# Kernel optimization log

Measured on AMD Instinct MI355X. Metric: run time of the kernel, lower is better.

The kernel has to match this reference:

```python
import jax, jax.numpy as jnp
import numpy as np
import math

C64 = jnp.complex64

def _fftconv_full(a, kern):
    # full linear convolution along last axis (complex), like scipy.signal.fftconvolve
    L = a.shape[-1] + kern.shape[0] - 1
    A = jnp.fft.fft(a, n=L, axis=-1)
    K = jnp.fft.fft(kern.astype(a.dtype), n=L)
    return jnp.fft.ifft(A * K, axis=-1)

def _centered_ifft(f):
    # out[shft] = ifft(f[shft]) * sqrt(N), shft = (arange(N)+fix(N/2)) % N
    N = f.shape[-1]
    shft = (np.arange(N) + int(np.fix(N / 2))) % N
    inv = np.argsort(shft)
    g = jnp.fft.ifft(f[..., shft], axis=-1) * math.sqrt(N)
    return g[..., inv].astype(f.dtype)

def _sincinterp(f):
    # zero-stuff by 2 then sinc-filter; returns length 2N-1 along last axis
    N = f.shape[-1]
    y = jnp.zeros(f.shape[:-1] + (2 * N - 1,), f.dtype).at[..., ::2].set(f)
    kern = jnp.asarray(np.sinc(np.arange(-(2 * N - 3), 2 * N - 2) / 2.0).astype(np.complex64))
    return _fftconv_full(y, kern)[..., 2 * N - 3: 4 * N - 4]

def _frft_chirp(f, a):
    # Ozaktas chirp-convolution discrete FrFT, valid for 0.5 <= a <= 1.5
    N = f.shape[-1]
    alpha = a * math.pi / 2
    tana2, sina = math.tan(alpha / 2), math.sin(alpha)
    fi = _sincinterp(f)                                   # [..., 2N-1]
    pad = jnp.zeros(f.shape[:-1] + (N - 1,), f.dtype)
    fp = jnp.concatenate([pad, fi, pad], axis=-1)         # [..., 4N-3]
    n = np.arange(-2 * N + 2, 2 * N - 1).astype(np.float64)
    chrp = jnp.asarray(np.exp(-1j * math.pi / N * tana2 / 4 * n ** 2).astype(np.complex64))
    fp = chrp * fp
    c = math.pi / N / sina / 4
    m = np.arange(-(4 * N - 4), 4 * N - 3).astype(np.float64)
    kern = jnp.asarray(np.exp(1j * c * m ** 2).astype(np.complex64))
    ret = _fftconv_full(fp, kern)[..., 4 * N - 4: 8 * N - 7] * math.sqrt(c / math.pi)
    ret = chrp * ret
    phase = np.complex64(np.exp(-1j * (1 - a) * math.pi / 4))
    return phase * ret[..., N - 1: 3 * N - 2: 2]          # [..., N]

def _frft_last(f, a):
    # torch branch logic for the a values used here: a=0.5 (fwd), a=-0.5 (inv)
    if a < 0.5:
        f = _centered_ifft(f)
        a = a + 1.0
    return _frft_chirp(f, a)

def _frft2d(x, a):
    t = _frft_last(x, a)                                  # rows: along W
    return jnp.swapaxes(_frft_last(jnp.swapaxes(t, -1, -2), a), -1, -2)  # cols: along H

def _c1x1(x, w, b=None):
    y = jnp.einsum('nchw,oc->nohw', x, w)
    return y if b is None else y + b[None, :, None, None]

def _c3x3(x, w, b):
    y = jax.lax.conv_general_dilated(x, w, (1, 1), 'SAME',
                                     dimension_numbers=('NCHW', 'OIHW', 'NCHW'))
    return y + b[None, :, None, None]

def _forward(x, conv1_w, mag_s_w, mag_s_b, mag_f_w, mag_f_b, mag_w, mag_b,
             pha_w, pha_b, conv_0_w, conv_0_b, conv_1_w, conv_1_b, conv2_w):
    angle = 0.5
    alpha = math.cos(angle * math.pi / 2)
    N, C, H, W = x.shape
    H1, W1 = int(H * alpha), int(W * alpha)
    x1 = _c1x1(x, conv1_w)                                # stride=1 -> downsample is identity
    C1, C0 = C // 4, C // 4 // 3
    x_0, x_05, x_1 = x1[:, :C0], x1[:, C0:C1 - C0], x1[:, C1 - C0:C1]
    h0, w0 = (H - H1) // 2, (W - W1) // 2
    mask1 = jnp.zeros((H, W), jnp.float32).at[h0:h0 + H1, w0:w0 + W1].set(1.0)
    mask2 = 1.0 - mask1
    # fractional Fourier branch
    Fre = _frft2d(x_05.astype(C64), angle)
    mag, pha = jnp.abs(Fre), jnp.angle(Fre)
    mag_out = _c1x1(_c3x3(mag * mask1, mag_s_w, mag_s_b) * mask1
                    + _c1x1(mag * mask2, mag_f_w, mag_f_b) * mask2, mag_w, mag_b)
    pha_out = _c1x1(pha, pha_w, pha_b)
    Fre_out = jax.lax.complex(mag_out * jnp.cos(pha_out), mag_out * jnp.sin(pha_out))
    ifrft = jnp.abs(_frft2d(Fre_out, -angle))
    # plain Fourier branch (conv_1 applied to both mag and pha, as in the source)
    fre = jnp.fft.rfft2(x_1)
    fm, fp = jnp.abs(fre), jnp.angle(fre)
    mo = _c1x1(fm, conv_1_w, conv_1_b)
    po = _c1x1(fp, conv_1_w, conv_1_b)
    x_1o = jnp.fft.irfft2(jax.lax.complex(mo * jnp.cos(po), mo * jnp.sin(po)), s=(H, W))
    x_0o = _c1x1(x_0, conv_0_w, conv_0_b)
    return _c1x1(jnp.concatenate([x_0o, ifrft, x_1o], axis=1), conv2_w)

def setup_inputs():
    key = jax.random.key(0)
    ks = jax.random.split(key, 16)
    N, C, H, W, Co = 4, 192, 128, 128, 192
    C1, C0 = C // 4, C // 4 // 3
    Cm = C1 - 2 * C0
    s = 0.05
    r = lambda k, sh: jax.random.normal(k, sh, jnp.float32)
    return {
        "x": r(ks[0], (N, C, H, W)),
        "conv1_w": r(ks[1], (C1, C)) * s,
        "mag_s_w": r(ks[2], (Cm, Cm, 3, 3)) * s, "mag_s_b": r(ks[3], (Cm,)) * s,
        "mag_f_w": r(ks[4], (Cm, Cm)) * s, "mag_f_b": r(ks[5], (Cm,)) * s,
        "mag_w": r(ks[6], (Cm, Cm)) * s, "mag_b": r(ks[7], (Cm,)) * s,
        "pha_w": r(ks[8], (Cm, Cm)) * s, "pha_b": r(ks[9], (Cm,)) * s,
        "conv_0_w": r(ks[10], (C0, C0)) * s, "conv_0_b": r(ks[11], (C0,)) * s,
        "conv_1_w": r(ks[12], (C0, C0)) * s, "conv_1_b": r(ks[13], (C0,)) * s,
        "conv2_w": r(ks[14], (Co, C1)) * s,
    }

def reference(x, conv1_w, mag_s_w, mag_s_b, mag_f_w, mag_f_b, mag_w, mag_b,
              pha_w, pha_b, conv_0_w, conv_0_b, conv_1_w, conv_1_b, conv2_w):
    return _forward(x, conv1_w, mag_s_w, mag_s_b, mag_f_w, mag_f_b, mag_w, mag_b,
                    pha_w, pha_b, conv_0_w, conv_0_b, conv_1_w, conv_1_b, conv2_w)
```

## Files before the change

### kernel.cpp

```cpp
#include <hip/hip_runtime.h>
#include <math.h>

#define PI_D 3.14159265358979323846
#define TWO_PI_F 6.2831853071795864f

__device__ __align__(16) float2 g_Mf [128*128];
__device__ __align__(16) float2 g_MfT[128*128];
__device__ __align__(16) float2 g_Mb [128*128];
__device__ __align__(16) float2 g_MbT[128*128];
__device__ __align__(16) float2 g_F  [128*128];
__device__ __align__(16) float2 g_IF [128*128];
__device__ __align__(16) float  g_x1 [4*48*16384];
__device__ __align__(16) float2 g_bufA[64*16384];
__device__ __align__(16) float2 g_bufB[64*16384];
__device__ __align__(16) float  g_mag[64*16384];
__device__ __align__(16) float  g_pha[64*16384];
__device__ __align__(16) float  g_m65[64*8320];
__device__ __align__(16) float  g_p65[64*8320];
__device__ __align__(16) float  g_t1 [64*16384];
__device__ __align__(16) float  g_t2 [64*16384];
__device__ __align__(16) float  g_t3 [64*8320];
__device__ __align__(16) float  g_t4 [64*8320];
__device__ __align__(16) float  g_cat[4*48*16384];

__device__ inline void build_A_body(int tid) {
    if (tid >= 128*128) return;
    int o = tid >> 7, m = tid & 127;
    const double chc = -PI_D/128.0 * tan(PI_D/8.0) * 0.25;
    const double c   =  PI_D/(512.0*sin(PI_D/4.0));
    const double inv2pi = 1.0/(2.0*PI_D);
    float sr, si;
    {
        int n1 = 2*m - 127, tt = 2*(o - m);
        double ang = chc*(double)(n1*n1) + c*(double)(tt*tt);
        double r = ang*inv2pi; r -= floor(r);
        float af = (float)(r*2.0*PI_D);
        float sn, cs; __sincosf(af, &sn, &cs);
        sr = cs; si = sn;
    }
    for (int j = 0; j < 127; ++j) {
        int q  = 2*j + 1;
        int n1 = q - 127, tt = 2*o - q, d = q - 2*m;
        double ang = chc*(double)(n1*n1) + c*(double)(tt*tt);
        double r = ang*inv2pi; r -= floor(r);
        float af = (float)(r*2.0*PI_D);
        float s = (((d-1)>>1) & 1) ? -2.0f : 2.0f;
        s /= (3.14159265358979f*(float)d);
        float sn, cs; __sincosf(af, &sn, &cs);
        sr += s*cs; si += s*sn;
    }
    int n2 = 2*o - 127;
    double ph = chc*(double)(n2*n2) - PI_D/8.0;
    double r = ph*inv2pi; r -= floor(r);
    float pf = (float)(r*2.0*PI_D);
    float scale = (float)sqrt(c/PI_D);
    float sn, cs; __sincosf(pf, &sn, &cs);
    float cr = cs*scale, ci = sn*scale;
    float2 v = make_float2(sr*cr - si*ci, sr*ci + si*cr);
    g_Mf[tid] = v;
    g_MfT[(m<<7) + o] = v;
    int p = (o*m) & 127;
    float ang2 = TWO_PI_F*(float)p/128.0f;
    float sn2, cs2; __sincosf(ang2, &sn2, &cs2);
    g_F[tid]  = make_float2(cs2, -sn2);
    g_IF[tid] = make_float2(cs2*0.0078125f, sn2*0.0078125f);
}

template<int LM>
__device__ inline void load_T4(float2* tr, const float* mp, const float* pp,
                               const float* Trl, int hh, int w4) {
    if (LM == 1) {
        float4 v = *(const float4*)(Trl + (hh<<7) + w4);
        tr[0] = make_float2(v.x, 0.f); tr[1] = make_float2(v.y, 0.f);
        tr[2] = make_float2(v.z, 0.f); tr[3] = make_float2(v.w, 0.f);
    } else if (LM == 2) {
#pragma unroll
        for (int i = 0; i < 4; ++i) {
            int idx = (hh<<7) + w4 + i;
            float m = mp[idx], ph = pp[idx];
            float sn, cs; __sincosf(ph, &sn, &cs);
            tr[i] = make_float2(m*cs, m*sn);
        }
    } else {
#pragma unroll
        for (int i = 0; i < 4; ++i) {
            int w = w4 + i;
            int h2 = hh, w2 = w; float sg = 1.f;
            if (w >= 65) { h2 = (128 - hh) & 127; w2 = 128 - w; sg = -1.f; }
            int idx = h2*65 + w2;
            float m = mp[idx], ph = pp[idx];
            float sn, cs; __sincosf(ph, &sn, &cs);
            tr[i] = make_float2(m*cs, sg*m*sn);
        }
    }
}

template<int LM>
__device__ inline void rmul_body(const float2* __restrict__ MT, const float* __restrict__ Trl,
                                 const float* __restrict__ mp_, const float* __restrict__ pp_,
                                 float2* __restrict__ out, int cstart,
                                 int p, int r0, int t, float2* Ssh, float2* Mch) {
    constexpr bool RS = (LM == 1);
    const float* Trp = nullptr; const float* mp = nullptr; const float* pp = nullptr;
    if (LM == 1) { int n = p >> 4, c = p & 15; Trp = Trl + ((long)(n*48 + cstart + c) << 14); }
    if (LM == 2) { mp = mp_ + ((long)p << 14); pp = pp_ + ((long)p << 14); }
    if (LM == 3) { mp = mp_ + (long)p*8320;   pp = pp_ + (long)p*8320; }
    for (int u = t; u < 512; u += 256) {
        int row = u >> 5, w4 = (u & 31) << 2;
        float2 tr4[4];
        load_T4<LM>(tr4, mp, pp, Trp, r0 + row, w4);
        float4* d = (float4*)&Ssh[(row << 7) + w4];
        d[0] = make_float4(tr4[0].x, tr4[0].y, tr4[1].x, tr4[1].y);
        d[1] = make_float4(tr4[2].x, tr4[2].y, tr4[3].x, tr4[3].y);
    }
    float2 acc[4][2] = {};
    int cq = t & 63, rp = t >> 6;
    for (int kc = 0; kc < 128; kc += 32) {
        __syncthreads();
        {
            const float4* Mg = (const float4*)(MT + (kc << 7));
            float4* Md = (float4*)Mch;
            for (int i = t; i < 2048; i += 256) Md[i] = Mg[i];
        }
        __syncthreads();
#pragma unroll
        for (int kk = 0; kk < 32; ++kk) {
            int k = kc + kk;
            float2 s[4], m[2];
#pragma unroll
            for (int i = 0; i < 4; ++i) s[i] = Ssh[(((rp<<2)+i) << 7) + k];
            m[0] = Mch[(kk << 7) + cq];
            m[1] = Mch[(kk << 7) + cq + 64];
#pragma unroll
            for (int i = 0; i < 4; ++i)
#pragma unroll
                for (int q = 0; q < 2; ++q) {
                    if (RS) {
                        acc[i][q].x = fmaf(s[i].x, m[q].x, acc[i][q].x);
                        acc[i][q].y = fmaf(s[i].x, m[q].y, acc[i][q].y);
                    } else {
                        acc[i][q].x = fmaf(s[i].x, m[q].x, acc[i][q].x);
                        acc[i][q].x = fmaf(-s[i].y, m[q].y, acc[i][q].x);
                        acc[i][q].y = fmaf(s[i].x, m[q].y, acc[i][q].y);
                        acc[i][q].y = fmaf(s[i].y, m[q].x, acc[i][q].y);
                    }
                }
        }
    }
    long base = ((long)p << 14);
#pragma unroll
    for (int i = 0; i < 4; ++i) {
        out[base + ((long)(r0 + (rp<<2) + i) << 7) + cq]      = acc[i][0];
        out[base + ((long)(r0 + (rp<<2) + i) << 7) + cq + 64] = acc[i][1];
    }
}

template<int EPI>
__device__ inline void lmul_body(const float2* __restrict__ A, const float2* __restrict__ in,
                                 float* __restrict__ o1, float* __restrict__ o2, int coff,
                                 int p, int j0, int t, float2* Ssh, float2* Tch) {
    const float2* T = in + ((long)p << 14);
    {
        const float4* Ag = (const float4*)(A + ((long)j0 << 7));
        float4* Sd = (float4*)Ssh;
        for (int i = t; i < 1024; i += 256) Sd[i] = Ag[i];
    }
    float2 acc[4][2] = {};
    int cq = t & 63, rp = t >> 6;
    for (int kc = 0; kc < 128; kc += 16) {
        __syncthreads();
        {
            const float4* Tg = (const float4*)(T + (kc << 7));
            float4* Td = (float4*)Tch;
            for (int i = t; i < 1024; i += 256) Td[i] = Tg[i];
        }
        __syncthreads();
#pragma unroll
        for (int kk = 0; kk < 16; ++kk) {
            int k = kc + kk;
            float2 s[4], m[2];
#pragma unroll
            for (int i = 0; i < 4; ++i) s[i] = Ssh[(((rp<<2)+i) << 7) + k];
            m[0] = Tch[(kk << 7) + cq];
            m[1] = Tch[(kk << 7) + cq + 64];
#pragma unroll
            for (int i = 0; i < 4; ++i)
#pragma unroll
                for (int q = 0; q < 2; ++q) {
                    if (EPI == 3) {
                        acc[i][q].x = fmaf(s[i].x, m[q].x, acc[i][q].x);
                        acc[i][q].x = fmaf(-s[i].y, m[q].y, acc[i][q].x);
                    } else {
                        acc[i][q].x = fmaf(s[i].x, m[q].x, acc[i][q].x);
                        acc[i][q].x = fmaf(-s[i].y, m[q].y, acc[i][q].x);
                        acc[i][q].y = fmaf(s[i].x, m[q].y, acc[i][q].y);
                        acc[i][q].y = fmaf(s[i].y, m[q].x, acc[i][q].y);
                    }
                }
        }
    }
#pragma unroll
    for (int i = 0; i < 4; ++i) {
#pragma unroll
        for (int q = 0; q < 2; ++q) {
            int jj = j0 + (rp<<2) + i;
            int ww = cq + (q<<6);
            float2 v = acc[i][q];
            if (EPI == 1) {
                long idx = ((long)p << 14) + ((long)jj << 7) + ww;
                o1[idx] = sqrtf(v.x*v.x + v.y*v.y);
                o2[idx] = atan2f(v.y, v.x);
            } else if (EPI == 2) {
                int n = p >> 4, c = p & 15;
                o1[((long)(n*48 + coff + c) << 14) + ((long)jj << 7) + ww] = sqrtf(v.x*v.x + v.y*v.y);
            } else if (EPI == 3) {
                int n = p >> 4, c = p & 15;
                o1[((long)(n*48 + coff + c) << 14) + ((long)jj << 7) + ww] = v.x;
            } else if (EPI == 4) {
                if (ww < 65) {
                    long idx = (long)p*8320 + jj*65 + ww;
                    o1[idx] = sqrtf(v.x*v.x + v.y*v.y);
                    o2[idx] = atan2f(v.y, v.x);
                }
            }
        }
    }
}

template<int LMA, int LMB>
__global__ __launch_bounds__(256, 3)
void k_rmul_dual(const float2* __restrict__ MTa, const float* __restrict__ TrlA,
                 const float* __restrict__ mpA, const float* __restrict__ ppA,
                 float2* __restrict__ outA, int cstartA,
                 const float2* __restrict__ MTb, const float* __restrict__ TrlB,
                 const float* __restrict__ mpB, const float* __restrict__ ppB,
                 float2* __restrict__ outB, int cstartB) {
    __shared__ float2 Ssh[16*128];
    __shared__ float2 Mch[32*128];
    __shared__ float2 W[128];
    int bx = blockIdx.x, by = blockIdx.y, t = threadIdx.x;
    if (bx >= 128) {
        int b = (bx - 128)*8 + by;
        if (b < 64) {
            if (t < 128) {
                float ang = TWO_PI_F*(float)t/128.0f;
                float sn, cs; __sincosf(ang, &sn, &cs);
                float invs = 0.08838834764831845f;
                W[t] = make_float2(cs*invs, sn*invs);
            }
            __syncthreads();
            int tid = b*256 + t;
            int o = tid >> 7, m = tid & 127;
            float sr = 0.f, si = 0.f;
            for (int r = 0; r < 128; ++r) {
                float2 a = g_Mf[(o<<7) + r];
                int k = ((r+64)*(m+64)) & 127;
                float2 w = W[k];
                sr += a.x*w.x - a.y*w.y;
                si += a.x*w.y + a.y*w.x;
            }
            float2 v = make_float2(sr, si);
            g_Mb[tid] = v;
            g_MbT[(m<<7) + o] = v;
        }
        return;
    }
    int p = bx & 63, r0 = by << 4;
    if (bx < 64) rmul_body<LMA>(MTa, TrlA, mpA, ppA, outA, cstartA, p, r0, t, Ssh, Mch);
    else         rmul_body<LMB>(MTb, TrlB, mpB, ppB, outB, cstartB, p, r0, t, Ssh, Mch);
}

template<int EPIA, int EPIB>
__global__ __launch_bounds__(256, 4)
void k_lmul_dual(const float2* __restrict__ Aa, const float2* __restrict__ inA,
                 float* __restrict__ o1A, float* __restrict__ o2A, int coffA,
                 const float2* __restrict__ Ab, const float2* __restrict__ inB,
                 float* __restrict__ o1B, float* __restrict__ o2B, int coffB) {
    __shared__ float2 Ssh[16*128];
    __shared__ float2 Tch[16*128];
    int bx = blockIdx.x, j0 = blockIdx.y << 4, t = threadIdx.x;
    int p = bx & 63;
    if (bx < 64) lmul_body<EPIA>(Aa, inA, o1A, o2A, coffA, p, j0, t, Ssh, Tch);
    else         lmul_body<EPIB>(Ab, inB, o1B, o2B, coffB, p, j0, t, Ssh, Tch);
}

template<int CIN, int COUT, int KSPLIT, int OSPLIT>
__device__ inline void wconv_body(const float* __restrict__ in, const float* __restrict__ wgt,
                                  const float* __restrict__ bias, float* __restrict__ out,
                                  int S, int Ctin, int cstart, int Ctout, int costart,
                                  int n, int sblk, float* red) {
    constexpr int OW = COUT / OSPLIT;
    constexpr int KC = CIN / KSPLIT;
    int t = threadIdx.x, lane = t & 63;
    int wv = __builtin_amdgcn_readfirstlane(t >> 6);
    int oq = wv / KSPLIT, kq = wv % KSPLIT;
    int s0 = sblk << 7;
    const float* inb = in + ((long)(n*Ctin + cstart + kq*KC))*S + s0 + (lane<<1);
    const float* wb  = wgt + (oq*OW)*CIN + kq*KC;
    float2 acc[OW];
#pragma unroll
    for (int j = 0; j < OW; ++j) acc[j] = make_float2(0.f, 0.f);
#pragma unroll 4
    for (int c = 0; c < KC; ++c) {
        float2 xv = *(const float2*)(inb + (long)c*S);
#pragma unroll
        for (int j = 0; j < OW; ++j) {
            float w = wb[j*CIN + c];
            acc[j].x = fmaf(w, xv.x, acc[j].x);
            acc[j].y = fmaf(w, xv.y, acc[j].y);
        }
    }
    if (KSPLIT == 1) {
#pragma unroll
        for (int j = 0; j < OW; ++j) {
            int o = oq*OW + j;
            float b = bias ? bias[o] : 0.f;
            *(float2*)(out + ((long)(n*Ctout + costart + o))*S + s0 + (lane<<1))
                = make_float2(acc[j].x + b, acc[j].y + b);
        }
    } else {
#pragma unroll
        for (int j = 0; j < OW; ++j) {
            int o = oq*OW + j;
            *(float2*)&red[((kq*COUT + o) << 7) + (lane<<1)] = acc[j];
        }
        __syncthreads();
        for (int idx = t; idx < COUT*64; idx += 256) {
            int o = idx >> 6, l2 = (idx & 63) << 1;
            float b = bias ? bias[o] : 0.f;
            float2 v = make_float2(b, b);
#pragma unroll
            for (int k2 = 0; k2 < KSPLIT; ++k2) {
                float2 r = *(const float2*)&red[((k2*COUT + o) << 7) + l2];
                v.x += r.x; v.y += r.y;
            }
            *(float2*)(out + ((long)(n*Ctout + costart + o))*S + s0 + l2) = v;
        }
    }
}

__global__ __launch_bounds__(256, 1)
void k_conv1_build(const float* __restrict__ x, const float* __restrict__ w,
                   float* __restrict__ x1) {
    __shared__ float red[2*48*128];
    if (blockIdx.z == 0) {
        wconv_body<192,48,2,2>(x, w, nullptr, x1, 16384, 192, 0, 48, 0,
                               blockIdx.y, blockIdx.x, red);
    } else {
        int b = blockIdx.y*gridDim.x + blockIdx.x;
        if (b < 64) build_A_body(b*256 + threadIdx.x);
    }
}

__global__ __launch_bounds__(256, 1)
void k_conv2(const float* __restrict__ in, const float* __restrict__ wgt,
             float* __restrict__ out) {
    __shared__ float red[1];
    wconv_body<48,192,1,4>(in, wgt, nullptr, out, 16384, 48, 0, 192, 0,
                           blockIdx.y, blockIdx.x, red);
}

__device__ inline void mix16b(const float* __restrict__ in, const float* __restrict__ w,
                              const float* __restrict__ b, float* __restrict__ out,
                              int Ctin, int S, int n, int s0) {
    int t = threadIdx.x, lane = t & 63;
    int oq = __builtin_amdgcn_readfirstlane(t >> 6);
    const float* inb = in + ((long)(n*Ctin))*S + s0 + (lane<<1);
    float2 xv[16];
#pragma unroll
    for (int c = 0; c < 16; ++c) xv[c] = *(const float2*)(inb + (long)c*S);
#pragma unroll
    for (int j = 0; j < 4; ++j) {
        int o = oq*4 + j;
        float bb = b ? b[o] : 0.f;
        float2 a = make_float2(bb, bb);
#pragma unroll
        for (int c = 0; c < 16; ++c) {
            float ww = w[o*16 + c];
            a.x = fmaf(ww, xv[c].x, a.x);
            a.y = fmaf(ww, xv[c].y, a.y);
        }
        *(float2*)(out + ((long)(n*Ctin + o))*S + s0 + (lane<<1)) = a;
    }
}

__device__ inline void maskconv_body(const float* __restrict__ mag, const float* __restrict__ ws3,
                                     const float* __restrict__ bs, const float* __restrict__ wf,
                                     const float* __restrict__ bf, const float* __restrict__ wm,
                                     const float* __restrict__ bm, float* __restrict__ out,
                                     int n, int tile, float (*patch)[324]) {
    int h0 = (tile >> 3) << 4, w0 = (tile & 7) << 4;
    int t = threadIdx.x;
    const float* magn = mag + ((long)n << 18);
    for (int idx = t; idx < 16*324; idx += 256) {
        int c = idx / 324, r = idx - c*324;
        int ph = r / 18, pw = r - ph*18;
        int gh = h0 - 1 + ph, gw = w0 - 1 + pw;
        float v = 0.f;
        if (gh >= 19 && gh < 109 && gw >= 19 && gw < 109)
            v = magn[(c<<14) + (gh<<7) + gw];
        patch[c][r] = v;
    }
    __syncthreads();
    int ty = t >> 4, tx = t & 15;
    int h = h0 + ty, w = w0 + tx;
    bool in1 = (h >= 19 && h < 109 && w >= 19 && w < 109);
    unsigned long long bal = __ballot(in1);
    float res[16];
    if (bal != 0ull) {
        float acc[16];
#pragma unroll
        for (int o = 0; o < 16; ++o) acc[o] = bs[o];
        for (int c = 0; c < 16; ++c) {
            float tap[9];
#pragma unroll
            for (int dh = 0; dh < 3; ++dh)
#pragma unroll
                for (int dw = 0; dw < 3; ++dw)
                    tap[dh*3+dw] = patch[c][(ty+dh)*18 + tx+dw];
            const float* wp = ws3 + c*9;
#pragma unroll
            for (int o = 0; o < 16; ++o)
#pragma unroll
                for (int k = 0; k < 9; ++k)
                    acc[o] = fmaf(wp[o*144 + k], tap[k], acc[o]);
        }
#pragma unroll
        for (int o = 0; o < 16; ++o) res[o] = acc[o];
    }
    if (bal != ~0ull) {
        float xv[16];
#pragma unroll
        for (int c = 0; c < 16; ++c) xv[c] = magn[(c<<14) + (h<<7) + w];
#pragma unroll
        for (int o = 0; o < 16; ++o) {
            float a = bf[o];
#pragma unroll
            for (int c = 0; c < 16; ++c) a = fmaf(wf[o*16 + c], xv[c], a);
            if (!in1) res[o] = a;
        }
    }
#pragma unroll
    for (int o2 = 0; o2 < 16; ++o2) {
        float a = bm[o2];
#pragma unroll
        for (int o = 0; o < 16; ++o)
            a = fmaf(wm[o2*16 + o], res[o], a);
        out[((long)((n<<4) + o2) << 14) + (h << 7) + w] = a;
    }
}

__global__ __launch_bounds__(256, 2)
void k_point(const float* __restrict__ mag, const float* __restrict__ ws3,
             const float* __restrict__ bs, const float* __restrict__ wf,
             const float* __restrict__ bf, const float* __restrict__ wm,
             const float* __restrict__ bm, float* __restrict__ t2,
             const float* __restrict__ pha, const float* __restrict__ pw,
             const float* __restrict__ pb, float* __restrict__ t1,
             const float* __restrict__ x1, const float* __restrict__ c0w,
             const float* __restrict__ c0b, float* __restrict__ cat,
             const float* __restrict__ m65, const float* __restrict__ p65,
             const float* __restrict__ c1w, const float* __restrict__ c1b,
             float* __restrict__ t3, float* __restrict__ t4) {
    __shared__ float patch[16][324];
    int b = blockIdx.x;
    if (b < 256) {
        maskconv_body(mag, ws3, bs, wf, bf, wm, bm, t2, b >> 6, b & 63, patch);
    } else if (b < 768) {
        int i = b - 256;
        mix16b(pha, pw, pb, t1, 16, 16384, i >> 7, (i & 127) << 7);
    } else if (b < 1280) {
        int i = b - 768;
        mix16b(x1, c0w, c0b, cat, 48, 16384, i >> 7, (i & 127) << 7);
    } else if (b < 1540) {
        int i = b - 1280;
        mix16b(m65, c1w, c1b, t3, 16, 8320, i / 65, (i % 65) << 7);
    } else {
        int i = b - 1540;
        mix16b(p65, c1w, c1b, t4, 16, 8320, i / 65, (i % 65) << 7);
    }
}

extern "C" void kernel_launch(void* const* d_in, const int* in_sizes, int n_in,
                              void* d_out, int out_size, void* d_ws, size_t ws_size,
                              hipStream_t stream) {
    (void)in_sizes; (void)n_in; (void)out_size; (void)d_ws; (void)ws_size;
    const float* x        = (const float*)d_in[0];
    const float* conv1_w  = (const float*)d_in[1];
    const float* mag_s_w  = (const float*)d_in[2];
    const float* mag_s_b  = (const float*)d_in[3];
    const float* mag_f_w  = (const float*)d_in[4];
    const float* mag_f_b  = (const float*)d_in[5];
    const float* mag_w_   = (const float*)d_in[6];
    const float* mag_b_   = (const float*)d_in[7];
    const float* pha_w_   = (const float*)d_in[8];
    const float* pha_b_   = (const float*)d_in[9];
    const float* conv_0_w = (const float*)d_in[10];
    const float* conv_0_b = (const float*)d_in[11];
    const float* conv_1_w = (const float*)d_in[12];
    const float* conv_1_b = (const float*)d_in[13];
    const float* conv2_w  = (const float*)d_in[14];
    float* outp = (float*)d_out;

    float2 *Mf, *MfT, *Mb, *MbT, *Fm, *IFm, *bufA, *bufB;
    float *x1, *mag, *pha, *m65, *p65, *t1, *t2, *t3, *t4, *cat;
    hipGetSymbolAddress((void**)&Mf,   HIP_SYMBOL(g_Mf));
    hipGetSymbolAddress((void**)&MfT,  HIP_SYMBOL(g_MfT));
    hipGetSymbolAddress((void**)&Mb,   HIP_SYMBOL(g_Mb));
    hipGetSymbolAddress((void**)&MbT,  HIP_SYMBOL(g_MbT));
    hipGetSymbolAddress((void**)&Fm,   HIP_SYMBOL(g_F));
    hipGetSymbolAddress((void**)&IFm,  HIP_SYMBOL(g_IF));
    hipGetSymbolAddress((void**)&bufA, HIP_SYMBOL(g_bufA));
    hipGetSymbolAddress((void**)&bufB, HIP_SYMBOL(g_bufB));
    hipGetSymbolAddress((void**)&x1,   HIP_SYMBOL(g_x1));
    hipGetSymbolAddress((void**)&mag,  HIP_SYMBOL(g_mag));
    hipGetSymbolAddress((void**)&pha,  HIP_SYMBOL(g_pha));
    hipGetSymbolAddress((void**)&m65,  HIP_SYMBOL(g_m65));
    hipGetSymbolAddress((void**)&p65,  HIP_SYMBOL(g_p65));
    hipGetSymbolAddress((void**)&t1,   HIP_SYMBOL(g_t1));
    hipGetSymbolAddress((void**)&t2,   HIP_SYMBOL(g_t2));
    hipGetSymbolAddress((void**)&t3,   HIP_SYMBOL(g_t3));
    hipGetSymbolAddress((void**)&t4,   HIP_SYMBOL(g_t4));
    hipGetSymbolAddress((void**)&cat,  HIP_SYMBOL(g_cat));

    dim3 bt(256, 1, 1);

    k_conv1_build<<<dim3(128,4,2), bt, 0, stream>>>(x, conv1_w, x1);

    k_rmul_dual<1,1><<<dim3(136,8), bt, 0, stream>>>(
        MfT, x1, nullptr, nullptr, bufA, 16,
        Fm,  x1, nullptr, nullptr, bufB, 32);

    k_lmul_dual<1,4><<<dim3(128,8), bt, 0, stream>>>(
        Mf, bufA, mag, pha, 0,
        Fm, bufB, m65, p65, 0);

    k_point<<<1800, bt, 0, stream>>>(mag, mag_s_w, mag_s_b, mag_f_w, mag_f_b,
                                     mag_w_, mag_b_, t2,
                                     pha, pha_w_, pha_b_, t1,
                                     x1, conv_0_w, conv_0_b, cat,
                                     m65, p65, conv_1_w, conv_1_b, t3, t4);

    k_rmul_dual<2,3><<<dim3(128,8), bt, 0, stream>>>(
        MbT, nullptr, t2, t1, bufA, 0,
        IFm, nullptr, t3, t4, bufB, 0);

    k_lmul_dual<2,3><<<dim3(128,8), bt, 0, stream>>>(
        Mb,  bufA, cat, nullptr, 16,
        IFm, bufB, cat, nullptr, 32);

    k_conv2<<<dim3(128,4), bt, 0, stream>>>(cat, conv2_w, outp);
}
```

Before: 337.9 us.

## Vectorize LDS loads in complex GEMM bodies, shrink M chunk, raise occupancy

Each thread now owns two adjacent output columns instead of two columns 64 apart. This lets the inner loops read two k-steps of S and the M/T tiles as float4 LDS loads, and lets outputs and epilogues be written as float4/float2 stores. The M chunk in the right-multiply kernel is halved from 32 to 16 rows, which cuts shared memory, and launch bounds go from 3 to 4 blocks per CU for more occupancy. The cost is twice as many barrier/load phases in rmul, possible LDS bank conflicts from the new strided float4 pattern, and tighter register limits.

```diff
diff --git a/kernel.cpp b/kernel.cpp
--- a/kernel.cpp
+++ b/kernel.cpp
@@ -95,6 +95,11 @@
     }
 }
 
+__device__ inline void cfma(float2& a, float sx, float sy, float mx, float my) {
+    a.x = fmaf(sx, mx, a.x); a.x = fmaf(-sy, my, a.x);
+    a.y = fmaf(sx, my, a.y); a.y = fmaf(sy, mx, a.y);
+}
+
 template<int LM>
 __device__ inline void rmul_body(const float2* __restrict__ MT, const float* __restrict__ Trl,
                                  const float* __restrict__ mp_, const float* __restrict__ pp_,
@@ -115,43 +120,47 @@
     }
     float2 acc[4][2] = {};
     int cq = t & 63, rp = t >> 6;
-    for (int kc = 0; kc < 128; kc += 32) {
+    for (int kc = 0; kc < 128; kc += 16) {
         __syncthreads();
         {
             const float4* Mg = (const float4*)(MT + (kc << 7));
             float4* Md = (float4*)Mch;
-            for (int i = t; i < 2048; i += 256) Md[i] = Mg[i];
+            for (int i = t; i < 1024; i += 256) Md[i] = Mg[i];
         }
         __syncthreads();
 #pragma unroll
-        for (int kk = 0; kk < 32; ++kk) {
-            int k = kc + kk;
-            float2 s[4], m[2];
-#pragma unroll
-            for (int i = 0; i < 4; ++i) s[i] = Ssh[(((rp<<2)+i) << 7) + k];
-            m[0] = Mch[(kk << 7) + cq];
-            m[1] = Mch[(kk << 7) + cq + 64];
+        for (int kk = 0; kk < 16; kk += 2) {
+            float4 s2[4];
 #pragma unroll
             for (int i = 0; i < 4; ++i)
-#pragma unroll
-                for (int q = 0; q < 2; ++q) {
-                    if (RS) {
-                        acc[i][q].x = fmaf(s[i].x, m[q].x, acc[i][q].x);
-                        acc[i][q].y = fmaf(s[i].x, m[q].y, acc[i][q].y);
-                    } else {
-                        acc[i][q].x = fmaf(s[i].x, m[q].x, acc[i][q].x);
-                        acc[i][q].x = fmaf(-s[i].y, m[q].y, acc[i][q].x);
-                        acc[i][q].y = fmaf(s[i].x, m[q].y, acc[i][q].y);
-                        acc[i][q].y = fmaf(s[i].y, m[q].x, acc[i][q].y);
-                    }
+                s2[i] = *(const float4*)&Ssh[(((rp<<2)+i) << 7) + kc + kk];
+            float4 m0 = *(const float4*)&Mch[(kk << 7) + (cq<<1)];
+            float4 m1 = *(const float4*)&Mch[((kk+1) << 7) + (cq<<1)];
+#pragma unroll
+            for (int i = 0; i < 4; ++i) {
+                if (RS) {
+                    acc[i][0].x = fmaf(s2[i].x, m0.x, acc[i][0].x);
+                    acc[i][0].y = fmaf(s2[i].x, m0.y, acc[i][0].y);
+                    acc[i][1].x = fmaf(s2[i].x, m0.z, acc[i][1].x);
+                    acc[i][1].y = fmaf(s2[i].x, m0.w, acc[i][1].y);
+                    acc[i][0].x = fmaf(s2[i].z, m1.x, acc[i][0].x);
+                    acc[i][0].y = fmaf(s2[i].z, m1.y, acc[i][0].y);
+                    acc[i][1].x = fmaf(s2[i].z, m1.z, acc[i][1].x);
+                    acc[i][1].y = fmaf(s2[i].z, m1.w, acc[i][1].y);
+                } else {
+                    cfma(acc[i][0], s2[i].x, s2[i].y, m0.x, m0.y);
+                    cfma(acc[i][1], s2[i].x, s2[i].y, m0.z, m0.w);
+                    cfma(acc[i][0], s2[i].z, s2[i].w, m1.x, m1.y);
+                    cfma(acc[i][1], s2[i].z, s2[i].w, m1.z, m1.w);
                 }
+            }
         }
     }
     long base = ((long)p << 14);
 #pragma unroll
     for (int i = 0; i < 4; ++i) {
-        out[base + ((long)(r0 + (rp<<2) + i) << 7) + cq]      = acc[i][0];
-        out[base + ((long)(r0 + (rp<<2) + i) << 7) + cq + 64] = acc[i][1];
+        float4* dst = (float4*)(out + base + ((long)(r0 + (rp<<2) + i) << 7) + (cq<<1));
+        *dst = make_float4(acc[i][0].x, acc[i][0].y, acc[i][1].x, acc[i][1].y);
     }
 }
 
@@ -176,59 +185,68 @@
         }
         __syncthreads();
 #pragma unroll
-        for (int kk = 0; kk < 16; ++kk) {
-            int k = kc + kk;
-            float2 s[4], m[2];
-#pragma unroll
-            for (int i = 0; i < 4; ++i) s[i] = Ssh[(((rp<<2)+i) << 7) + k];
-            m[0] = Tch[(kk << 7) + cq];
-            m[1] = Tch[(kk << 7) + cq + 64];
+        for (int kk = 0; kk < 16; kk += 2) {
+            float4 s2[4];
 #pragma unroll
             for (int i = 0; i < 4; ++i)
-#pragma unroll
-                for (int q = 0; q < 2; ++q) {
-                    if (EPI == 3) {
-                        acc[i][q].x = fmaf(s[i].x, m[q].x, acc[i][q].x);
-                        acc[i][q].x = fmaf(-s[i].y, m[q].y, acc[i][q].x);
-                    } else {
-                        acc[i][q].x = fmaf(s[i].x, m[q].x, acc[i][q].x);
-                        acc[i][q].x = fmaf(-s[i].y, m[q].y, acc[i][q].x);
-                        acc[i][q].y = fmaf(s[i].x, m[q].y, acc[i][q].y);
-                        acc[i][q].y = fmaf(s[i].y, m[q].x, acc[i][q].y);
-                    }
-                }
-        }
-    }
-#pragma unroll
-    for (int i = 0; i < 4; ++i) {
-#pragma unroll
-        for (int q = 0; q < 2; ++q) {
-            int jj = j0 + (rp<<2) + i;
-            int ww = cq + (q<<6);
-            float2 v = acc[i][q];
-            if (EPI == 1) {
-                long idx = ((long)p << 14) + ((long)jj << 7) + ww;
-                o1[idx] = sqrtf(v.x*v.x + v.y*v.y);
-                o2[idx] = atan2f(v.y, v.x);
-            } else if (EPI == 2) {
-                int n = p >> 4, c = p & 15;
-                o1[((long)(n*48 + coff + c) << 14) + ((long)jj << 7) + ww] = sqrtf(v.x*v.x + v.y*v.y);
-            } else if (EPI == 3) {
-                int n = p >> 4, c = p & 15;
-                o1[((long)(n*48 + coff + c) << 14) + ((long)jj << 7) + ww] = v.x;
-            } else if (EPI == 4) {
-                if (ww < 65) {
-                    long idx = (long)p*8320 + jj*65 + ww;
-                    o1[idx] = sqrtf(v.x*v.x + v.y*v.y);
-                    o2[idx] = atan2f(v.y, v.x);
+                s2[i] = *(const float4*)&Ssh[(((rp<<2)+i) << 7) + kc + kk];
+            float4 m0 = *(const float4*)&Tch[(kk << 7) + (cq<<1)];
+            float4 m1 = *(const float4*)&Tch[((kk+1) << 7) + (cq<<1)];
+#pragma unroll
+            for (int i = 0; i < 4; ++i) {
+                if (EPI == 3) {
+                    acc[i][0].x = fmaf(s2[i].x, m0.x, acc[i][0].x);
+                    acc[i][0].x = fmaf(-s2[i].y, m0.y, acc[i][0].x);
+                    acc[i][1].x = fmaf(s2[i].x, m0.z, acc[i][1].x);
+                    acc[i][1].x = fmaf(-s2[i].y, m0.w, acc[i][1].x);
+                    acc[i][0].x = fmaf(s2[i].z, m1.x, acc[i][0].x);
+                    acc[i][0].x = fmaf(-s2[i].w, m1.y, acc[i][0].x);
+                    acc[i][1].x = fmaf(s2[i].z, m1.z, acc[i][1].x);
+                    acc[i][1].x = fmaf(-s2[i].w, m1.w, acc[i][1].x);
+                } else {
+                    cfma(acc[i][0], s2[i].x, s2[i].y, m0.x, m0.y);
+                    cfma(acc[i][1], s2[i].x, s2[i].y, m0.z, m0.w);
+                    cfma(acc[i][0], s2[i].z, s2[i].w, m1.x, m1.y);
+                    cfma(acc[i][1], s2[i].z, s2[i].w, m1.z, m1.w);
                 }
             }
         }
     }
+#pragma unroll
+    for (int i = 0; i < 4; ++i) {
+        int jj = j0 + (rp<<2) + i;
+        int ww0 = cq << 1;
+        float2 v0 = acc[i][0], v1 = acc[i][1];
+        if (EPI == 1) {
+            long idx = ((long)p << 14) + ((long)jj << 7) + ww0;
+            *(float2*)&o1[idx] = make_float2(sqrtf(v0.x*v0.x + v0.y*v0.y),
+                                             sqrtf(v1.x*v1.x + v1.y*v1.y));
+            *(float2*)&o2[idx] = make_float2(atan2f(v0.y, v0.x), atan2f(v1.y, v1.x));
+        } else if (EPI == 2) {
+            int n = p >> 4, c = p & 15;
+            long idx = ((long)(n*48 + coff + c) << 14) + ((long)jj << 7) + ww0;
+            *(float2*)&o1[idx] = make_float2(sqrtf(v0.x*v0.x + v0.y*v0.y),
+                                             sqrtf(v1.x*v1.x + v1.y*v1.y));
+        } else if (EPI == 3) {
+            int n = p >> 4, c = p & 15;
+            long idx = ((long)(n*48 + coff + c) << 14) + ((long)jj << 7) + ww0;
+            *(float2*)&o1[idx] = make_float2(v0.x, v1.x);
+        } else if (EPI == 4) {
+            if (ww0 < 65) {
+                long idx = (long)p*8320 + jj*65 + ww0;
+                o1[idx] = sqrtf(v0.x*v0.x + v0.y*v0.y);
+                o2[idx] = atan2f(v0.y, v0.x);
+                if (ww0 + 1 < 65) {
+                    o1[idx+1] = sqrtf(v1.x*v1.x + v1.y*v1.y);
+                    o2[idx+1] = atan2f(v1.y, v1.x);
+                }
+            }
+        }
+    }
 }
 
 template<int LMA, int LMB>
-__global__ __launch_bounds__(256, 3)
+__global__ __launch_bounds__(256, 4)
 void k_rmul_dual(const float2* __restrict__ MTa, const float* __restrict__ TrlA,
                  const float* __restrict__ mpA, const float* __restrict__ ppA,
                  float2* __restrict__ outA, int cstartA,
@@ -236,7 +254,7 @@
                  const float* __restrict__ mpB, const float* __restrict__ ppB,
                  float2* __restrict__ outB, int cstartB) {
     __shared__ float2 Ssh[16*128];
-    __shared__ float2 Mch[32*128];
+    __shared__ float2 Mch[16*128];
     __shared__ float2 W[128];
     int bx = blockIdx.x, by = blockIdx.y, t = threadIdx.x;
     if (bx >= 128) {
```

New measurement: 331.7 us. Within noise of the previous version (-1.8%).
